# Optimization experiments

Hardware: AMD Instinct MI355X
Metric: run time of the kernel (lower is better)

Reference implementation:

```python
import jax, jax.numpy as jnp
import numpy as np

D_MODEL = 1024
D_HEAD = 64

def setup_inputs() -> dict:
    key = jax.random.key(0)
    kx, kk, kq, kv = jax.random.split(key, 4)
    s = D_MODEL ** -0.5
    return {
        "x": jax.random.normal(kx, (4, 4096, D_MODEL), dtype=jnp.float32),
        "Wk": jax.random.normal(kk, (D_MODEL, D_HEAD), dtype=jnp.float32) * s,
        "Wq": jax.random.normal(kq, (D_MODEL, D_HEAD), dtype=jnp.float32) * s,
        "Wv": jax.random.normal(kv, (D_MODEL, D_HEAD), dtype=jnp.float32) * s,
    }

def reference(x, Wk, Wq, Wv):
    # x: [B, T, d_model]; Wk/Wq/Wv: [d_model, d_head]
    B, T, _ = x.shape
    d_head = Wk.shape[1]
    k = x @ Wk  # [B, T, d_head]
    q = x @ Wq
    v = x @ Wv
    scores = jnp.einsum("btd,bsd->bts", q, k) * (d_head ** -0.5)  # [B, T, T]
    causal = jnp.tril(jnp.ones((T, T), dtype=bool))
    scores = jnp.where(causal, scores, -jnp.inf)
    weights = jax.nn.softmax(scores, axis=-1)
    return jnp.einsum("bts,bsd->btd", weights, v)
```

## Files before the change

kernel.cpp:

```cpp
#include <hip/hip_runtime.h>

typedef __attribute__((ext_vector_type(8))) short bf16x8;
typedef __attribute__((ext_vector_type(4))) float f32x4;

#define DI __device__ __forceinline__

DI unsigned short f2bf(float f) {
    unsigned int u = __builtin_bit_cast(unsigned int, f);
    u += 0x7fff + ((u >> 16) & 1);
    return (unsigned short)(u >> 16);
}

DI unsigned int cvtpk(float lo, float hi) {
    unsigned int r;
    asm("v_cvt_pk_bf16_f32 %0, %1, %2" : "=v"(r) : "v"(lo), "v"(hi));
    return r;
}

DI void gl_lds16(const void* g, void* l) {
    __builtin_amdgcn_global_load_lds(
        (const __attribute__((address_space(1))) unsigned int*)g,
        (__attribute__((address_space(3))) unsigned int*)l, 16, 0, 0);
}

#define WAITCNT(n) asm volatile("s_waitcnt vmcnt(" #n ")" ::: "memory")

__global__ __launch_bounds__(256) void wt_kernel(
    const float* __restrict__ Wk, const float* __restrict__ Wq,
    const float* __restrict__ Wv, unsigned short* __restrict__ Wt)
{
    __shared__ float ws[64][65];
    const int m = blockIdx.x >> 4, kc = blockIdx.x & 15;
    const float* W = (m == 0) ? Wq : (m == 1) ? Wk : Wv;
    const float scale = (m == 0) ? 0.18033688011112042f : 1.0f;
    const int tid = threadIdx.x;
    #pragma unroll
    for (int r = 0; r < 16; ++r) {
        int idx = r * 256 + tid;
        ws[idx >> 6][idx & 63] = W[(kc * 64 + (idx >> 6)) * 64 + (idx & 63)] * scale;
    }
    __syncthreads();
    const int c = tid >> 2, k4 = (tid & 3) * 16;
    bf16x8 o0, o1;
    #pragma unroll
    for (int j = 0; j < 8; ++j) o0[j] = (short)f2bf(ws[k4 + j][c]);
    #pragma unroll
    for (int j = 0; j < 8; ++j) o1[j] = (short)f2bf(ws[k4 + 8 + j][c]);
    unsigned short* dst = Wt + ((size_t)m * 64 + c) * 1024 + kc * 64 + k4;
    *(bf16x8*)dst = o0;
    *(bf16x8*)(dst + 8) = o1;
}

__global__ __launch_bounds__(256) void proj_kernel(
    const float* __restrict__ x, const unsigned short* __restrict__ Wt,
    unsigned short* __restrict__ qw, unsigned short* __restrict__ kw,
    unsigned short* __restrict__ vT)
{
    __shared__ char LDSx[3][8192];
    __shared__ char LDSb[3][6144];

    const int tid = threadIdx.x;
    const int w = tid >> 6, l = tid & 63;
    const int xr = l & 15, lg = l >> 4;
    const int rb = blockIdx.x & 255, ch = blockIdx.x >> 8;
    const int row0 = rb * 64;

    const char* xsrc = (const char*)x + (size_t)row0 * 4096;
    const char* Wtb = (const char*)Wt;

    const int xrow_l = l >> 3, xcb = (l & 7) * 16;
    const int brow_l = l >> 2, bcb = (l & 3) * 16;

    auto stage = [&](int nb, int s) {
        #pragma unroll
        for (int c = 0; c < 4; ++c) {
            const int ci = w + 4 * c;
            if (ci < 8) {
                const int row = ci * 8 + xrow_l;
                const int sw = (row & 7) << 4;
                gl_lds16(xsrc + (size_t)row * 4096 + (size_t)s * 128 + (xcb ^ sw),
                         LDSx[nb] + ci * 1024);
            } else if (ci < 14) {
                const int c8 = ci - 8;
                const int r = c8 * 16 + brow_l;
                const int sw = ((r >> 1) & 3) << 4;
                const int wtrow = (r >> 5) * 64 + ch * 32 + (r & 31);
                gl_lds16(Wtb + (size_t)wtrow * 2048 + (size_t)s * 64 + (bcb ^ sw),
                         LDSb[nb] + c8 * 1024);
            }
        }
    };

    f32x4 acc[3][2];
    #pragma unroll
    for (int m = 0; m < 3; ++m)
        #pragma unroll
        for (int tt = 0; tt < 2; ++tt) { f32x4 z = {0.f,0.f,0.f,0.f}; acc[m][tt] = z; }

    const int Rw = w * 16 + xr;
    const int swx = (Rw & 7) << 4;

    auto compute = [&](int pb) {
        float4 va = *(const float4*)(LDSx[pb] + Rw * 128 + ((32 * lg) ^ swx));
        float4 vb = *(const float4*)(LDSx[pb] + Rw * 128 + ((32 * lg + 16) ^ swx));
        bf16x8 a;
        a[0] = (short)f2bf(va.x); a[1] = (short)f2bf(va.y);
        a[2] = (short)f2bf(va.z); a[3] = (short)f2bf(va.w);
        a[4] = (short)f2bf(vb.x); a[5] = (short)f2bf(vb.y);
        a[6] = (short)f2bf(vb.z); a[7] = (short)f2bf(vb.w);
        __builtin_amdgcn_s_setprio(1);
        #pragma unroll
        for (int m = 0; m < 3; ++m)
            #pragma unroll
            for (int tt = 0; tt < 2; ++tt) {
                const int rB = m * 32 + tt * 16 + xr;
                bf16x8 bfr = *(const bf16x8*)(LDSb[pb] + rB * 64 +
                                ((16 * lg) ^ (((rB >> 1) & 3) << 4)));
                acc[m][tt] = __builtin_amdgcn_mfma_f32_16x16x32_bf16(a, bfr, acc[m][tt], 0, 0, 0);
            }
        __builtin_amdgcn_s_setprio(0);
    };

    stage(0, 0); stage(1, 1);

    int cb = 0, nb = 2;
    for (int s = 0; s < 32; ++s) {
        if (s == 31) { WAITCNT(0); }
        else if (w < 2) { WAITCNT(4); }
        else { WAITCNT(3); }
        __builtin_amdgcn_sched_barrier(0);
        __builtin_amdgcn_s_barrier();
        if (s + 2 < 32) stage(nb, s + 2);
        compute(cb);
        cb = (cb == 2) ? 0 : cb + 1;
        nb = (nb == 2) ? 0 : nb + 1;
    }

    const int bb = row0 >> 12;
    #pragma unroll
    for (int tt = 0; tt < 2; ++tt) {
        const int col = ch * 32 + tt * 16 + xr;
        unsigned short pv4[4];
        #pragma unroll
        for (int i = 0; i < 4; ++i) {
            const int grow = row0 + w * 16 + 4 * lg + i;
            qw[(size_t)grow * 64 + col] = f2bf(acc[0][tt][i]);
            kw[(size_t)grow * 64 + col] = f2bf(acc[1][tt][i]);
            pv4[i] = f2bf(acc[2][tt][i]);
        }
        const int lr0 = (row0 & 4095) + w * 16 + 4 * lg;
        *(uint2*)&vT[((size_t)bb * 64 + col) * 4096 + lr0] = *(const uint2*)pv4;
    }
}

__global__ __launch_bounds__(256) void attn_kernel(
    const unsigned short* __restrict__ qw, const unsigned short* __restrict__ kw,
    const unsigned short* __restrict__ vT,
    unsigned short* __restrict__ POb, float* __restrict__ Pl)
{
    __shared__ __align__(16) unsigned short Kb[2][4096];
    __shared__ __align__(16) unsigned short Vb[2][4096];
    __shared__ __align__(16) unsigned short Ps[4][16][64];

    const int id = blockIdx.x;
    const int qb = 63 - (id & 63);
    const int b  = (id >> 6) & 3;
    const int c  = id >> 8;
    if (c * 8 > qb) return;

    const int tid = threadIdx.x;
    const int w = tid >> 6, l = tid & 63;
    const int xr = l & 15, g = l >> 4;

    const int t0 = c * 8;
    const int rem0 = qb + 1 - t0;
    const int tcnt = rem0 < 8 ? rem0 : 8;
    const size_t base = (size_t)b * 4096;
    const int qrow = qb * 64 + w * 16;
    const int myrow = qrow + xr;

    bf16x8 aq[2];
    #pragma unroll
    for (int h = 0; h < 2; ++h)
        aq[h] = *(const bf16x8*)(qw + (base + myrow) * 64 + 32 * h + 8 * g);

    const int wo0 = w * 2048, wo1 = wo0 + 1024;
    const int o0 = wo0 + 16 * l, o1 = wo1 + 16 * l;
    const int k0sw = (o0 & ~127) | ((o0 & 127) ^ (((o0 >> 7) & 7) << 4));
    const int k1sw = (o1 & ~127) | ((o1 & 127) ^ (((o1 >> 7) & 7) << 4));
    const size_t v0sw = (size_t)(o0 >> 7) * 8192 + ((o0 & 127) ^ (((o0 >> 7) & 7) << 4));
    const size_t v1sw = (size_t)(o1 >> 7) * 8192 + ((o1 & 127) ^ (((o1 >> 7) & 7) << 4));
    const char* kwb  = (const char*)kw + base * 128;
    const char* vtb0 = (const char*)vT + (size_t)b * 64 * 8192;

    auto stage = [&](int bi, int it) {
        const char* kt = kwb + (size_t)it * 8192;
        gl_lds16(kt + k0sw, (char*)Kb[bi] + wo0);
        gl_lds16(kt + k1sw, (char*)Kb[bi] + wo1);
        const char* vt = vtb0 + (size_t)it * 128;
        gl_lds16(vt + v0sw, (char*)Vb[bi] + wo0);
        gl_lds16(vt + v1sw, (char*)Vb[bi] + wo1);
    };

    f32x4 accO[4];
    #pragma unroll
    for (int t = 0; t < 4; ++t) { f32x4 z = {0.f,0.f,0.f,0.f}; accO[t] = z; }
    float lsum = 0.f;

    const int swz = (xr & 7) << 4;
    char* const psrow = (char*)Ps + w * 2048 + xr * 128;

    stage(0, t0);
    if (tcnt > 1) stage(1, t0 + 1);

    for (int tt = 0; tt < tcnt; ++tt) {
        const int it = t0 + tt;
        const int bi = tt & 1;
        if (tt + 1 < tcnt) { WAITCNT(4); } else { WAITCNT(0); }
        __builtin_amdgcn_sched_barrier(0);
        __builtin_amdgcn_s_barrier();

        const char* kbase = (const char*)Kb[bi];
        f32x4 s[4];
        __builtin_amdgcn_s_setprio(1);
        #pragma unroll
        for (int t = 0; t < 4; ++t) {
            f32x4 z = {0.f,0.f,0.f,0.f};
            s[t] = z;
            #pragma unroll
            for (int h = 0; h < 2; ++h) {
                bf16x8 ak = *(const bf16x8*)(kbase + (xr + 16 * t) * 128 + ((64 * h + 16 * g) ^ swz));
                s[t] = __builtin_amdgcn_mfma_f32_16x16x32_bf16(ak, aq[h], s[t], 0, 0, 0);
            }
        }
        __builtin_amdgcn_s_setprio(0);

        if (it == qb) {
            #pragma unroll
            for (int t = 0; t < 4; ++t)
                #pragma unroll
                for (int i = 0; i < 4; ++i) {
                    const int key = it * 64 + 16 * t + 4 * g + i;
                    if (key > myrow) s[t][i] = -1e30f;
                }
        }

        #pragma unroll
        for (int t = 0; t < 4; ++t)
            #pragma unroll
            for (int i = 0; i < 4; ++i)
                s[t][i] = exp2f(s[t][i]);

        {
            float a0 = (s[0][0] + s[0][1]) + (s[0][2] + s[0][3]);
            float a1 = (s[1][0] + s[1][1]) + (s[1][2] + s[1][3]);
            float a2 = (s[2][0] + s[2][1]) + (s[2][2] + s[2][3]);
            float a3 = (s[3][0] + s[3][1]) + (s[3][2] + s[3][3]);
            lsum += (a0 + a1) + (a2 + a3);
        }

        #pragma unroll
        for (int t = 0; t < 4; ++t) {
            uint2 uu;
            uu.x = cvtpk(s[t][0], s[t][1]);
            uu.y = cvtpk(s[t][2], s[t][3]);
            *(uint2*)(psrow + ((32 * t + 8 * g) ^ swz)) = uu;
        }

        bf16x8 pa[2];
        #pragma unroll
        for (int h = 0; h < 2; ++h)
            pa[h] = *(const bf16x8*)(psrow + ((16 * g + 64 * h) ^ swz));
        const char* vbase = (const char*)Vb[bi];
        __builtin_amdgcn_s_setprio(1);
        #pragma unroll
        for (int t = 0; t < 4; ++t)
            #pragma unroll
            for (int h = 0; h < 2; ++h) {
                bf16x8 av = *(const bf16x8*)(vbase + (16 * t + xr) * 128 + ((64 * h + 16 * g) ^ swz));
                accO[t] = __builtin_amdgcn_mfma_f32_16x16x32_bf16(av, pa[h], accO[t], 0, 0, 0);
            }
        __builtin_amdgcn_s_setprio(0);

        __builtin_amdgcn_s_barrier();
        if (tt + 2 < tcnt) stage(bi, it + 2);
    }

    lsum += __shfl_xor(lsum, 16, 64);
    lsum += __shfl_xor(lsum, 32, 64);

    const size_t prow = (size_t)(b * 8 + c) * 4096 + qrow;
    #pragma unroll
    for (int t = 0; t < 4; ++t) {
        uint2 uu;
        uu.x = cvtpk(accO[t][0], accO[t][1]);
        uu.y = cvtpk(accO[t][2], accO[t][3]);
        *(uint2*)&POb[(prow + xr) * 64 + 16 * t + 4 * g] = uu;
    }
    if (l < 16) Pl[prow + l] = lsum;
}

__global__ __launch_bounds__(256) void merge_kernel(
    const unsigned short* __restrict__ POb, const float* __restrict__ Pl,
    float* __restrict__ out)
{
    const int gid = blockIdx.x * 256 + threadIdx.x;
    const int r = gid >> 2;
    const int c0 = (gid & 3) * 16;
    const int b = r >> 12, lr = r & 4095;
    const int nc = (lr >> 9) + 1;

    float L = 0.f;
    #pragma unroll
    for (int ci = 0; ci < 8; ++ci)
        if (ci < nc) L += Pl[(size_t)(b * 8 + ci) * 4096 + lr];
    const float rL = 1.0f / L;

    float acc[16];
    #pragma unroll
    for (int j = 0; j < 16; ++j) acc[j] = 0.f;

    #pragma unroll
    for (int ci = 0; ci < 8; ++ci) {
        if (ci < nc) {
            const unsigned short* p = POb + ((size_t)(b * 8 + ci) * 4096 + lr) * 64 + c0;
            uint4 u0 = *(const uint4*)p;
            uint4 u1 = *(const uint4*)(p + 8);
            const unsigned int us[8] = {u0.x, u0.y, u0.z, u0.w, u1.x, u1.y, u1.z, u1.w};
            #pragma unroll
            for (int k = 0; k < 8; ++k) {
                acc[2 * k]     += __builtin_bit_cast(float, us[k] << 16);
                acc[2 * k + 1] += __builtin_bit_cast(float, us[k] & 0xFFFF0000u);
            }
        }
    }
    float* op = out + (size_t)r * 64 + c0;
    #pragma unroll
    for (int j = 0; j < 4; ++j) {
        float4 v;
        v.x = acc[4 * j]     * rL;
        v.y = acc[4 * j + 1] * rL;
        v.z = acc[4 * j + 2] * rL;
        v.w = acc[4 * j + 3] * rL;
        *(float4*)(op + 4 * j) = v;
    }
}

extern "C" void kernel_launch(void* const* d_in, const int* in_sizes, int n_in,
                              void* d_out, int out_size, void* d_ws, size_t ws_size,
                              hipStream_t stream) {
    const float* x  = (const float*)d_in[0];
    const float* Wk = (const float*)d_in[1];
    const float* Wq = (const float*)d_in[2];
    const float* Wv = (const float*)d_in[3];
    float* out = (float*)d_out;

    char* wsb = (char*)d_ws;
    unsigned short* POb = (unsigned short*)wsb;
    float* Pl = (float*)(wsb + (size_t)17 * 1024 * 1024);
    unsigned short* Wt = (unsigned short*)(wsb + (size_t)24 * 1024 * 1024);
    unsigned short* qw = Wt + (size_t)3 * 64 * 1024;
    unsigned short* kw = qw + (size_t)16384 * 64;
    unsigned short* vT = kw + (size_t)16384 * 64;

    hipLaunchKernelGGL(wt_kernel, dim3(48), dim3(256), 0, stream, Wk, Wq, Wv, Wt);
    hipLaunchKernelGGL(proj_kernel, dim3(512), dim3(256), 0, stream, x, Wt, qw, kw, vT);
    hipLaunchKernelGGL(attn_kernel, dim3(2048), dim3(256), 0, stream, qw, kw, vT, POb, Pl);
    hipLaunchKernelGGL(merge_kernel, dim3(256), dim3(256), 0, stream, POb, Pl, out);
}
```

Baseline: 64.89 us.

## Use hardware bf16 pack and raw v_exp, widen merge kernel parallelism

In the projection kernel, the software round-to-bf16 conversions of x tiles and V outputs become packed v_cvt_pk_bf16_f32 instructions. In the attention softmax, exp2f is replaced with a raw v_exp_f32 inline asm, which drops the compiler's range handling. The merge kernel now has each thread handle 8 columns instead of 16 and launches twice as many blocks, which raises parallelism for the final reduction. These cut ALU work in the projection and attention inner loops, at the risk of slightly different rounding or denormal behaviour.

```diff
diff --git a/kernel.cpp b/kernel.cpp
--- a/kernel.cpp
+++ b/kernel.cpp
@@ -14,6 +14,12 @@
 DI unsigned int cvtpk(float lo, float hi) {
     unsigned int r;
     asm("v_cvt_pk_bf16_f32 %0, %1, %2" : "=v"(r) : "v"(lo), "v"(hi));
+    return r;
+}
+
+DI float fexp2(float x) {
+    float r;
+    asm("v_exp_f32 %0, %1" : "=v"(r) : "v"(x));
     return r;
 }
 
@@ -103,11 +109,10 @@
     auto compute = [&](int pb) {
         float4 va = *(const float4*)(LDSx[pb] + Rw * 128 + ((32 * lg) ^ swx));
         float4 vb = *(const float4*)(LDSx[pb] + Rw * 128 + ((32 * lg + 16) ^ swx));
-        bf16x8 a;
-        a[0] = (short)f2bf(va.x); a[1] = (short)f2bf(va.y);
-        a[2] = (short)f2bf(va.z); a[3] = (short)f2bf(va.w);
-        a[4] = (short)f2bf(vb.x); a[5] = (short)f2bf(vb.y);
-        a[6] = (short)f2bf(vb.z); a[7] = (short)f2bf(vb.w);
+        uint4 au;
+        au.x = cvtpk(va.x, va.y); au.y = cvtpk(va.z, va.w);
+        au.z = cvtpk(vb.x, vb.y); au.w = cvtpk(vb.z, vb.w);
+        bf16x8 a = __builtin_bit_cast(bf16x8, au);
         __builtin_amdgcn_s_setprio(1);
         #pragma unroll
         for (int m = 0; m < 3; ++m)
@@ -140,16 +145,17 @@
     #pragma unroll
     for (int tt = 0; tt < 2; ++tt) {
         const int col = ch * 32 + tt * 16 + xr;
-        unsigned short pv4[4];
         #pragma unroll
         for (int i = 0; i < 4; ++i) {
             const int grow = row0 + w * 16 + 4 * lg + i;
             qw[(size_t)grow * 64 + col] = f2bf(acc[0][tt][i]);
             kw[(size_t)grow * 64 + col] = f2bf(acc[1][tt][i]);
-            pv4[i] = f2bf(acc[2][tt][i]);
-        }
+        }
+        uint2 pv;
+        pv.x = cvtpk(acc[2][tt][0], acc[2][tt][1]);
+        pv.y = cvtpk(acc[2][tt][2], acc[2][tt][3]);
         const int lr0 = (row0 & 4095) + w * 16 + 4 * lg;
-        *(uint2*)&vT[((size_t)bb * 64 + col) * 4096 + lr0] = *(const uint2*)pv4;
+        *(uint2*)&vT[((size_t)bb * 64 + col) * 4096 + lr0] = pv;
     }
 }
 
@@ -248,8 +254,10 @@
         #pragma unroll
         for (int t = 0; t < 4; ++t)
             #pragma unroll
-            for (int i = 0; i < 4; ++i)
-                s[t][i] = exp2f(s[t][i]);
+            for (int i = 0; i < 4; ++i) {
+                float v = s[t][i];
+                s[t][i] = fexp2(v);
+            }
 
         {
             float a0 = (s[0][0] + s[0][1]) + (s[0][2] + s[0][3]);
@@ -305,8 +313,8 @@
     float* __restrict__ out)
 {
     const int gid = blockIdx.x * 256 + threadIdx.x;
-    const int r = gid >> 2;
-    const int c0 = (gid & 3) * 16;
+    const int r = gid >> 3;
+    const int c0 = (gid & 7) * 8;
     const int b = r >> 12, lr = r & 4095;
     const int nc = (lr >> 9) + 1;
 
@@ -316,34 +324,29 @@
         if (ci < nc) L += Pl[(size_t)(b * 8 + ci) * 4096 + lr];
     const float rL = 1.0f / L;
 
-    float acc[16];
-    #pragma unroll
-    for (int j = 0; j < 16; ++j) acc[j] = 0.f;
+    float acc[8];
+    #pragma unroll
+    for (int j = 0; j < 8; ++j) acc[j] = 0.f;
 
     #pragma unroll
     for (int ci = 0; ci < 8; ++ci) {
         if (ci < nc) {
             const unsigned short* p = POb + ((size_t)(b * 8 + ci) * 4096 + lr) * 64 + c0;
-            uint4 u0 = *(const uint4*)p;
-            uint4 u1 = *(const uint4*)(p + 8);
-            const unsigned int us[8] = {u0.x, u0.y, u0.z, u0.w, u1.x, u1.y, u1.z, u1.w};
-            #pragma unroll
-            for (int k = 0; k < 8; ++k) {
+            uint4 u = *(const uint4*)p;
+            const unsigned int us[4] = {u.x, u.y, u.z, u.w};
+            #pragma unroll
+            for (int k = 0; k < 4; ++k) {
                 acc[2 * k]     += __builtin_bit_cast(float, us[k] << 16);
                 acc[2 * k + 1] += __builtin_bit_cast(float, us[k] & 0xFFFF0000u);
             }
         }
     }
     float* op = out + (size_t)r * 64 + c0;
-    #pragma unroll
-    for (int j = 0; j < 4; ++j) {
-        float4 v;
-        v.x = acc[4 * j]     * rL;
-        v.y = acc[4 * j + 1] * rL;
-        v.z = acc[4 * j + 2] * rL;
-        v.w = acc[4 * j + 3] * rL;
-        *(float4*)(op + 4 * j) = v;
-    }
+    float4 v0, v1;
+    v0.x = acc[0] * rL; v0.y = acc[1] * rL; v0.z = acc[2] * rL; v0.w = acc[3] * rL;
+    v1.x = acc[4] * rL; v1.y = acc[5] * rL; v1.z = acc[6] * rL; v1.w = acc[7] * rL;
+    *(float4*)op = v0;
+    *(float4*)(op + 4) = v1;
 }
 
 extern "C" void kernel_launch(void* const* d_in, const int* in_sizes, int n_in,
@@ -366,5 +369,5 @@
     hipLaunchKernelGGL(wt_kernel, dim3(48), dim3(256), 0, stream, Wk, Wq, Wv, Wt);
     hipLaunchKernelGGL(proj_kernel, dim3(512), dim3(256), 0, stream, x, Wt, qw, kw, vT);
     hipLaunchKernelGGL(attn_kernel, dim3(2048), dim3(256), 0, stream, qw, kw, vT, POb, Pl);
-    hipLaunchKernelGGL(merge_kernel, dim3(256), dim3(256), 0, stream, POb, Pl, out);
-}
+    hipLaunchKernelGGL(merge_kernel, dim3(512), dim3(256), 0, stream, POb, Pl, out);
+}
```

Result: faster. 59.29 us (median of 3 runs) (-8.6%).
